# Optimization experiments

Hardware: AMD Instinct MI355X
Metric: run time of the kernel (lower is better)

## Reference

```python
import jax, jax.numpy as jnp
import numpy as np

SCALE = 0.1
TEMP = 1.0
LN_EPS = 1e-6
NORM_EPS = 1e-12  # torch F.normalize eps

def setup_inputs() -> dict:
    key = jax.random.key(0)
    k1, = jax.random.split(key, 1)
    x = jax.random.normal(k1, (8192, 512), dtype=jnp.float32)
    gamma = jnp.ones((512,), dtype=jnp.float32)
    beta = jnp.zeros((512,), dtype=jnp.float32)
    return {"x": x, "gamma": gamma, "beta": beta}

def reference(x, gamma, beta):
    # L2-normalize rows (torch F.normalize semantics: x / max(||x||, eps))
    norm = jnp.maximum(jnp.linalg.norm(x, axis=1, keepdims=True), NORM_EPS)
    xn = x / norm                                   # [N, d]
    sim = (xn @ xn.T) / TEMP                        # [N, N]
    # dual_norm: row softmax + column softmax
    sim = jax.nn.softmax(sim, axis=1) + jax.nn.softmax(sim, axis=0)
    x_neg = sim @ x                                 # [N, d]
    y = x - SCALE * x_neg
    # LayerNorm over last dim, eps=1e-6
    mean = jnp.mean(y, axis=-1, keepdims=True)
    var = jnp.mean(jnp.square(y - mean), axis=-1, keepdims=True)
    out = (y - mean) * jax.lax.rsqrt(var + LN_EPS) * gamma + beta
    return out
```

## Files before the change

kernel.cpp:

```cpp
#include <hip/hip_runtime.h>
#include <math.h>

#define NN 8192
#define DD 512

constexpr float SCALE_C = 0.1f;
constexpr float LN_EPS_C = 1e-6f;
constexpr float NORM_EPS_C = 1e-12f;
constexpr float CBIG = 32768.0f;
constexpr float INV_CBIG = 1.0f / 32768.0f;

typedef __attribute__((ext_vector_type(8))) short bf16x8;
typedef __attribute__((ext_vector_type(4))) float f32x4;

#define MFMA16(a, b, c) __builtin_amdgcn_mfma_f32_16x16x32_bf16((a), (b), (c), 0, 0, 0)
#define MFMA8(a, b, c)                                                        \
  __builtin_amdgcn_mfma_f32_16x16x32_fp8_fp8((long)(a), (long)(b), (c), 0, 0, 0)

#define GLL16(g, l)                                                        \
  __builtin_amdgcn_global_load_lds(                                        \
      (const __attribute__((address_space(1))) unsigned int*)(g),          \
      (__attribute__((address_space(3))) unsigned int*)(l), 16, 0, 0)

#define WAITV4() asm volatile("s_waitcnt vmcnt(4)" ::: "memory")
#define WAITV0() asm volatile("s_waitcnt vmcnt(0)" ::: "memory")
#define WAITLGKM0() asm volatile("s_waitcnt lgkmcnt(0)" ::: "memory")
#define FENCE() asm volatile("" ::: "memory")
#define BAR() __builtin_amdgcn_s_barrier()

__device__ inline unsigned short f2bf(float f) {
  unsigned int u = __builtin_bit_cast(unsigned int, f);
  unsigned int r = (u + 0x7FFFu + ((u >> 16) & 1u)) >> 16;
  return (unsigned short)r;
}

__device__ inline unsigned int f2fp8n(float f) {
  unsigned int a = __builtin_bit_cast(unsigned int, f);
  unsigned int r = a + 0x7FFFFu + ((a >> 20) & 1u);
  return (r >> 20) - 960u;
}

__device__ inline unsigned int f2fp8(float f) {
  unsigned int u = __builtin_bit_cast(unsigned int, f);
  unsigned int s = (u >> 24) & 0x80u;
  unsigned int a = u & 0x7fffffffu;
  if (a >= 0x3C800000u) {
    unsigned int r = a + 0x7FFFFu + ((a >> 20) & 1u);
    return s | ((r >> 20) - 960u);
  }
  float af = __builtin_bit_cast(float, a);
  return s | (unsigned int)(int)rintf(af * 512.0f);
}

__device__ inline float fp82f(unsigned int b) {
  return __builtin_bit_cast(float, (b + 960u) << 20);
}

__global__ __launch_bounds__(128) void k_prep(const float* __restrict__ x,
                                              unsigned short* __restrict__ xnb) {
  const int row = blockIdx.x;
  const int t = threadIdx.x;
  float4 v = ((const float4*)(x + (size_t)row * DD))[t];
  float ss = v.x * v.x + v.y * v.y + v.z * v.z + v.w * v.w;
#pragma unroll
  for (int off = 32; off; off >>= 1) ss += __shfl_down(ss, off);
  __shared__ float red[2];
  if ((t & 63) == 0) red[t >> 6] = ss;
  __syncthreads();
  float rn = 1.0f / fmaxf(sqrtf(red[0] + red[1]), NORM_EPS_C);
  ushort4 o;
  o.x = f2bf(v.x * rn);
  o.y = f2bf(v.y * rn);
  o.z = f2bf(v.z * rn);
  o.w = f2bf(v.w * rn);
  ((ushort4*)(xnb + (size_t)row * DD))[t] = o;
}

__global__ __launch_bounds__(256) void k_tr(const float* __restrict__ x,
                                            unsigned char* __restrict__ xT8) {
  __shared__ unsigned char T8[64][68];
  const int j0 = blockIdx.x * 64;
  const int d0 = blockIdx.y * 64;
  const int t = threadIdx.x;
#pragma unroll
  for (int q = 0; q < 4; ++q) {
    int f = t + q * 256;
    int r = f >> 4, c4 = f & 15;
    float4 v = *(const float4*)&x[(size_t)(j0 + r) * DD + d0 + c4 * 4];
    unsigned int w = f2fp8(v.x) | (f2fp8(v.y) << 8) | (f2fp8(v.z) << 16) |
                     (f2fp8(v.w) << 24);
    *(unsigned int*)&T8[r][c4 * 4] = w;
  }
  __syncthreads();
  {
    const int d = t >> 2, j16 = t & 3;
    unsigned int w[4];
#pragma unroll
    for (int p = 0; p < 4; ++p) {
      w[p] = (unsigned int)T8[j16 * 16 + p * 4 + 0][d] |
             ((unsigned int)T8[j16 * 16 + p * 4 + 1][d] << 8) |
             ((unsigned int)T8[j16 * 16 + p * 4 + 2][d] << 16) |
             ((unsigned int)T8[j16 * 16 + p * 4 + 3][d] << 24);
    }
    uint4 o = make_uint4(w[0], w[1], w[2], w[3]);
    *(uint4*)&xT8[(size_t)(d0 + d) * NN + j0 + j16 * 16] = o;
  }
}

__global__ __launch_bounds__(256, 4) void k_rowsumE(const unsigned short* __restrict__ xnb,
                                                    float* __restrict__ lpart,
                                                    unsigned char* __restrict__ E8) {
  __shared__ __align__(16) unsigned char POOL[36864];
  __shared__ float red[4][64];
  __shared__ float red2[4][64];

  int b = blockIdx.x, bi = 0;
  while (b >= 64 - bi) { b -= 64 - bi; ++bi; }
  const int bj = bi + b;
  const int i0 = bi * 128, j0 = bj * 128;
  const int diag = (bi == bj);

  const int t = threadIdx.x;
  const int w = t >> 6, l = t & 63;
  const int lr = l & 15, lg = l >> 4;
  const int wr = w >> 1, wc = w & 1;
  const int r0 = w * 16 + (l >> 2);
  const int clog = (l & 3) ^ ((r0 >> 1) & 3);
  const unsigned short* gA = xnb + (size_t)(i0 + r0) * DD + clog * 8;
  const unsigned short* gB = xnb + (size_t)(j0 + r0) * DD + clog * 8;

#define RS_STAGE(s, koff)                                                        \
  do {                                                                           \
    GLL16(gA + (koff), (unsigned short*)(POOL + (s) * 16384) + w * 512);         \
    GLL16(gA + (size_t)64 * DD + (koff),                                         \
          (unsigned short*)(POOL + (s) * 16384 + 4096) + w * 512);               \
    GLL16(gB + (koff), (unsigned short*)(POOL + (s) * 16384 + 8192) + w * 512);  \
    GLL16(gB + (size_t)64 * DD + (koff),                                         \
          (unsigned short*)(POOL + (s) * 16384 + 12288) + w * 512);              \
  } while (0)

  RS_STAGE(0, 0);
  RS_STAGE(1, 32);

  f32x4 acc[4][4] = {};
  for (int ks = 0; ks < 16; ++ks) {
    if (ks + 1 < 16) { WAITV4(); } else { WAITV0(); }
    BAR(); FENCE();
    const char* AS = (const char*)(POOL + (ks & 1) * 16384);
    const char* BS = AS + 8192;
    bf16x8 af[4], bv[4];
#pragma unroll
    for (int fm = 0; fm < 4; ++fm) {
      const int row = wr * 64 + fm * 16 + lr;
      af[fm] = *(const bf16x8*)(AS + row * 64 + ((lg ^ ((row >> 1) & 3)) << 4));
    }
#pragma unroll
    for (int fn = 0; fn < 4; ++fn) {
      const int row = wc * 64 + fn * 16 + lr;
      bv[fn] = *(const bf16x8*)(BS + row * 64 + ((lg ^ ((row >> 1) & 3)) << 4));
    }
    WAITLGKM0();
    BAR(); FENCE();
    if (ks + 2 < 16) RS_STAGE(ks & 1, (size_t)(ks + 2) * 32);
#pragma unroll
    for (int fm = 0; fm < 4; ++fm)
#pragma unroll
      for (int fn = 0; fn < 4; ++fn)
        acc[fm][fn] = MFMA16(af[fm], bv[fn], acc[fm][fn]);
  }

  unsigned int ebw[4][4];
  float rsum[4][4] = {};
  float csum[4] = {};
#pragma unroll
  for (int fm = 0; fm < 4; ++fm)
#pragma unroll
    for (int fn = 0; fn < 4; ++fn) {
      unsigned int pw = 0;
#pragma unroll
      for (int rr = 0; rr < 4; ++rr) {
        float e = __expf(acc[fm][fn][rr]);
        rsum[fm][rr] += e;
        csum[fn] += e;
        pw |= f2fp8n(e) << (8 * rr);
      }
      ebw[fm][fn] = pw;
    }

#pragma unroll
  for (int fm = 0; fm < 4; ++fm)
#pragma unroll
    for (int rr = 0; rr < 4; ++rr) {
      float s = rsum[fm][rr];
#pragma unroll
      for (int off = 1; off < 16; off <<= 1) s += __shfl_xor(s, off);
      if (lr == 0) red[w][fm * 16 + lg * 4 + rr] = s;
    }
  if (!diag) {
#pragma unroll
    for (int fn = 0; fn < 4; ++fn) {
      float cs = csum[fn];
      cs += __shfl_xor(cs, 16);
      cs += __shfl_xor(cs, 32);
      if (lg == 0) red2[w][fn * 16 + lr] = cs;
    }
  }

  unsigned char(*Et)[144] = (unsigned char(*)[144])POOL;
  unsigned char(*Et2)[144] = (unsigned char(*)[144])(POOL + 18432);
#pragma unroll
  for (int fm = 0; fm < 4; ++fm)
#pragma unroll
    for (int fn = 0; fn < 4; ++fn) {
#pragma unroll
      for (int rr = 0; rr < 4; ++rr)
        Et[wr * 64 + fm * 16 + lg * 4 + rr][wc * 64 + fn * 16 + lr] =
            (unsigned char)((ebw[fm][fn] >> (8 * rr)) & 0xffu);
      if (!diag)
        *(unsigned int*)&Et2[wc * 64 + fn * 16 + lr][wr * 64 + fm * 16 + lg * 4] =
            ebw[fm][fn];
    }
  __syncthreads();
  {
    unsigned char* dst = E8 + ((size_t)(bi * 64 + bj) << 14);
#pragma unroll
    for (int q = 0; q < 4; ++q) {
      const int f = t + q * 256;
      *(uint4*)(dst + f * 16) = *(const uint4*)&Et[f >> 3][(f & 7) * 16];
    }
    if (!diag) {
      unsigned char* dst2 = E8 + ((size_t)(bj * 64 + bi) << 14);
#pragma unroll
      for (int q = 0; q < 4; ++q) {
        const int f = t + q * 256;
        *(uint4*)(dst2 + f * 16) = *(const uint4*)&Et2[f >> 3][(f & 7) * 16];
      }
    }
  }
  if (t < 128) {
    const int wrx = t >> 6, idx = t & 63;
    lpart[(size_t)bj * NN + i0 + t] = red[2 * wrx][idx] + red[2 * wrx + 1][idx];
  } else if (!diag) {
    const int c = t - 128;
    const int wcx = c >> 6, idx = c & 63;
    lpart[(size_t)bi * NN + j0 + c] = red2[wcx][idx] + red2[2 + wcx][idx];
  }
}

__global__ __launch_bounds__(256) void k_recip(const float* __restrict__ lpart,
                                               float* __restrict__ rl) {
  const int i = blockIdx.x * 256 + threadIdx.x;
  float s = 0.f;
  for (int c = 0; c < 64; ++c) s += lpart[(size_t)c * NN + i];
  rl[i] = CBIG / s;
}

__global__ __launch_bounds__(256) void k_scale(unsigned char* __restrict__ P,
                                               const float* __restrict__ rl) {
  const long long total = (long long)NN * NN / 16;
  const long long stride = (long long)gridDim.x * 256;
  for (long long u = (long long)blockIdx.x * 256 + threadIdx.x; u < total; u += stride) {
    const long long byte = u * 16;
    const int tile = (int)(byte >> 14);
    const int within = (int)(byte & 16383);
    const int i = ((tile >> 6) << 7) + (within >> 7);
    const int j0 = ((tile & 63) << 7) + (within & 127);
    unsigned char* p = P + byte;
    uint4 v = *(const uint4*)p;
    const float rli = rl[i];
    float rlj[16];
#pragma unroll
    for (int q = 0; q < 4; ++q) {
      float4 r4 = *(const float4*)(rl + j0 + q * 4);
      rlj[q * 4 + 0] = r4.x; rlj[q * 4 + 1] = r4.y;
      rlj[q * 4 + 2] = r4.z; rlj[q * 4 + 3] = r4.w;
    }
    unsigned int wsrc[4] = {v.x, v.y, v.z, v.w};
    unsigned int wdst[4];
#pragma unroll
    for (int q = 0; q < 4; ++q) {
      unsigned int in = wsrc[q], out = 0;
#pragma unroll
      for (int k = 0; k < 4; ++k) {
        float e = fp82f((in >> (8 * k)) & 0xffu);
        out |= f2fp8n(e * (rli + rlj[q * 4 + k])) << (8 * k);
      }
      wdst[q] = out;
    }
    *(uint4*)p = make_uint4(wdst[0], wdst[1], wdst[2], wdst[3]);
  }
}

__global__ __launch_bounds__(256, 4) void k_pv3(const unsigned char* __restrict__ P8,
                                                const unsigned char* __restrict__ xT8,
                                                unsigned short* __restrict__ parts) {
  __shared__ __align__(16) unsigned char As[2][8192];
  __shared__ __align__(16) unsigned char Bs[2][8192];
  const int i0 = blockIdx.x * 128;
  const int n0 = blockIdx.y * 128;
  const int z = blockIdx.z;
  const int t = threadIdx.x;
  const int w = t >> 6, l = t & 63;
  const int lr = l & 15, lg = l >> 4;
  const int wr = w >> 1, wc = w & 1;
  const int r0 = w * 16 + (l >> 2);
  const int clog = (l & 3) ^ ((r0 >> 1) & 3);
  const unsigned char* Abase = P8 + ((size_t)((i0 >> 7) * 64 + z * 16) << 14) +
                               r0 * 128 + clog * 16;
  const unsigned char* gB = xT8 + (size_t)(n0 + r0) * NN + z * 2048 + clog * 16;

#define PV_STAGE(s, koff)                                                      \
  do {                                                                         \
    const unsigned char* a_ = Abase + (((koff) >> 7) << 14) + ((koff) & 127);  \
    GLL16(a_, &As[s][w * 1024]);                                               \
    GLL16(a_ + 8192, &As[s][4096 + w * 1024]);                                 \
    GLL16(gB + (koff), &Bs[s][w * 1024]);                                      \
    GLL16(gB + (size_t)64 * NN + (koff), &Bs[s][4096 + w * 1024]);             \
  } while (0)

  PV_STAGE(0, 0);
  PV_STAGE(1, 64);

  f32x4 acc[4][4] = {};
  for (int ks = 0; ks < 32; ++ks) {
    if (ks + 1 < 32) { WAITV4(); } else { WAITV0(); }
    BAR(); FENCE();
    const char* AS = (const char*)&As[ks & 1][0];
    const char* BS = (const char*)&Bs[ks & 1][0];
    unsigned long long af[4][2], bv[4][2];
#pragma unroll
    for (int fm = 0; fm < 4; ++fm) {
      const int row = wr * 64 + fm * 16 + lr;
      const int swz = (row >> 1) & 3;
#pragma unroll
      for (int kk = 0; kk < 2; ++kk) {
        int off = row * 64 + (((kk * 2 + (lg >> 1)) ^ swz) << 4) + ((lg & 1) << 3);
        af[fm][kk] = *(const unsigned long long*)(AS + off);
      }
    }
#pragma unroll
    for (int fn = 0; fn < 4; ++fn) {
      const int row = wc * 64 + fn * 16 + lr;
      const int swz = (row >> 1) & 3;
#pragma unroll
      for (int kk = 0; kk < 2; ++kk) {
        int off = row * 64 + (((kk * 2 + (lg >> 1)) ^ swz) << 4) + ((lg & 1) << 3);
        bv[fn][kk] = *(const unsigned long long*)(BS + off);
      }
    }
    WAITLGKM0();
    BAR(); FENCE();
    if (ks + 2 < 32) PV_STAGE(ks & 1, (ks + 2) * 64);
#pragma unroll
    for (int kk = 0; kk < 2; ++kk)
#pragma unroll
      for (int fm = 0; fm < 4; ++fm)
#pragma unroll
        for (int fn = 0; fn < 4; ++fn)
          acc[fm][fn] = MFMA8(af[fm][kk], bv[fn][kk], acc[fm][fn]);
  }
  unsigned short* dst = parts + (size_t)z * NN * DD;
#pragma unroll
  for (int fm = 0; fm < 4; ++fm)
#pragma unroll
    for (int fn = 0; fn < 4; ++fn)
#pragma unroll
      for (int rr = 0; rr < 4; ++rr)
        dst[(size_t)(i0 + wr * 64 + fm * 16 + lg * 4 + rr) * DD + n0 + wc * 64 +
            fn * 16 + lr] = f2bf(acc[fm][fn][rr] * INV_CBIG);
}

__global__ __launch_bounds__(128) void k_ln(const float* __restrict__ x,
                                            float* __restrict__ out,
                                            const unsigned short* __restrict__ parts,
                                            const float* __restrict__ gamma,
                                            const float* __restrict__ beta) {
  const int row = blockIdx.x;
  const int t = threadIdx.x;
  float4 p = make_float4(0.f, 0.f, 0.f, 0.f);
#pragma unroll
  for (int s = 0; s < 4; ++s) {
    ushort4 q = ((const ushort4*)(parts + (size_t)s * NN * DD + (size_t)row * DD))[t];
    p.x += __builtin_bit_cast(float, (unsigned int)q.x << 16);
    p.y += __builtin_bit_cast(float, (unsigned int)q.y << 16);
    p.z += __builtin_bit_cast(float, (unsigned int)q.z << 16);
    p.w += __builtin_bit_cast(float, (unsigned int)q.w << 16);
  }
  float4 xv = ((const float4*)(x + (size_t)row * DD))[t];
  float4 y;
  y.x = xv.x - SCALE_C * p.x;
  y.y = xv.y - SCALE_C * p.y;
  y.z = xv.z - SCALE_C * p.z;
  y.w = xv.w - SCALE_C * p.w;
  float sum = y.x + y.y + y.z + y.w;
#pragma unroll
  for (int off = 32; off; off >>= 1) sum += __shfl_down(sum, off);
  __shared__ float ra[2], rb[2];
  if ((t & 63) == 0) ra[t >> 6] = sum;
  __syncthreads();
  float mean = (ra[0] + ra[1]) * (1.0f / DD);
  float d0 = y.x - mean, d1 = y.y - mean, d2 = y.z - mean, d3 = y.w - mean;
  float vs = d0 * d0 + d1 * d1 + d2 * d2 + d3 * d3;
#pragma unroll
  for (int off = 32; off; off >>= 1) vs += __shfl_down(vs, off);
  if ((t & 63) == 0) rb[t >> 6] = vs;
  __syncthreads();
  float rstd = rsqrtf((rb[0] + rb[1]) * (1.0f / DD) + LN_EPS_C);
  float4 g4 = ((const float4*)gamma)[t];
  float4 b4 = ((const float4*)beta)[t];
  float4 o;
  o.x = d0 * rstd * g4.x + b4.x;
  o.y = d1 * rstd * g4.y + b4.y;
  o.z = d2 * rstd * g4.z + b4.z;
  o.w = d3 * rstd * g4.w + b4.w;
  ((float4*)(out + (size_t)row * DD))[t] = o;
}

extern "C" void kernel_launch(void* const* d_in, const int* in_sizes, int n_in,
                              void* d_out, int out_size, void* d_ws, size_t ws_size,
                              hipStream_t stream) {
  const float* x = (const float*)d_in[0];
  const float* gamma = (const float*)d_in[1];
  const float* beta = (const float*)d_in[2];
  float* out = (float*)d_out;

  unsigned short* xnb = (unsigned short*)d_ws;
  unsigned char* xT8 = (unsigned char*)(xnb + (size_t)NN * DD);
  float* lpart = (float*)(xT8 + (size_t)NN * DD);
  float* rl = lpart + (size_t)64 * NN;
  unsigned short* parts = (unsigned short*)(rl + NN);
  unsigned char* E8 = (unsigned char*)(parts + (size_t)4 * NN * DD);

  k_prep<<<NN, 128, 0, stream>>>(x, xnb);
  k_tr<<<dim3(NN / 64, DD / 64), 256, 0, stream>>>(x, xT8);
  k_rowsumE<<<2080, 256, 0, stream>>>(xnb, lpart, E8);
  k_recip<<<NN / 256, 256, 0, stream>>>(lpart, rl);
  k_scale<<<4096, 256, 0, stream>>>(E8, rl);
  k_pv3<<<dim3(64, 4, 4), 256, 0, stream>>>(E8, xT8, parts);
  k_ln<<<NN, 128, 0, stream>>>(x, out, parts, gamma, beta);
}
```

Baseline: 162.8 us.

## Triple-buffer LDS pipeline with one barrier per step, MFMA priority, block swizzle

```diff
diff --git a/kernel.cpp b/kernel.cpp
--- a/kernel.cpp
+++ b/kernel.cpp
@@ -24,7 +24,6 @@
 
 #define WAITV4() asm volatile("s_waitcnt vmcnt(4)" ::: "memory")
 #define WAITV0() asm volatile("s_waitcnt vmcnt(0)" ::: "memory")
-#define WAITLGKM0() asm volatile("s_waitcnt lgkmcnt(0)" ::: "memory")
 #define FENCE() asm volatile("" ::: "memory")
 #define BAR() __builtin_amdgcn_s_barrier()
 
@@ -107,14 +106,15 @@
   }
 }
 
-__global__ __launch_bounds__(256, 4) void k_rowsumE(const unsigned short* __restrict__ xnb,
+__global__ __launch_bounds__(256, 3) void k_rowsumE(const unsigned short* __restrict__ xnb,
                                                     float* __restrict__ lpart,
                                                     unsigned char* __restrict__ E8) {
-  __shared__ __align__(16) unsigned char POOL[36864];
+  __shared__ __align__(16) unsigned char POOL[49152];
   __shared__ float red[4][64];
   __shared__ float red2[4][64];
 
-  int b = blockIdx.x, bi = 0;
+  int b = (blockIdx.x & 7) * 260 + (blockIdx.x >> 3);
+  int bi = 0;
   while (b >= 64 - bi) { b -= 64 - bi; ++bi; }
   const int bj = bi + b;
   const int i0 = bi * 128, j0 = bj * 128;
@@ -144,9 +144,11 @@
 
   f32x4 acc[4][4] = {};
   for (int ks = 0; ks < 16; ++ks) {
-    if (ks + 1 < 16) { WAITV4(); } else { WAITV0(); }
+    WAITV4();
     BAR(); FENCE();
-    const char* AS = (const char*)(POOL + (ks & 1) * 16384);
+    const int kn = (ks + 2 < 16) ? ks + 2 : 15;
+    RS_STAGE((ks + 2) % 3, (size_t)kn * 32);
+    const char* AS = (const char*)(POOL + (ks % 3) * 16384);
     const char* BS = AS + 8192;
     bf16x8 af[4], bv[4];
 #pragma unroll
@@ -159,15 +161,15 @@
       const int row = wc * 64 + fn * 16 + lr;
       bv[fn] = *(const bf16x8*)(BS + row * 64 + ((lg ^ ((row >> 1) & 3)) << 4));
     }
-    WAITLGKM0();
-    BAR(); FENCE();
-    if (ks + 2 < 16) RS_STAGE(ks & 1, (size_t)(ks + 2) * 32);
+    __builtin_amdgcn_s_setprio(1);
 #pragma unroll
     for (int fm = 0; fm < 4; ++fm)
 #pragma unroll
       for (int fn = 0; fn < 4; ++fn)
         acc[fm][fn] = MFMA16(af[fm], bv[fn], acc[fm][fn]);
-  }
+    __builtin_amdgcn_s_setprio(0);
+  }
+  BAR(); FENCE();
 
   unsigned int ebw[4][4];
   float rsum[4][4] = {};
@@ -291,11 +293,10 @@
   }
 }
 
-__global__ __launch_bounds__(256, 4) void k_pv3(const unsigned char* __restrict__ P8,
+__global__ __launch_bounds__(256, 3) void k_pv3(const unsigned char* __restrict__ P8,
                                                 const unsigned char* __restrict__ xT8,
                                                 unsigned short* __restrict__ parts) {
-  __shared__ __align__(16) unsigned char As[2][8192];
-  __shared__ __align__(16) unsigned char Bs[2][8192];
+  __shared__ __align__(16) unsigned char POOL[49152];
   const int i0 = blockIdx.x * 128;
   const int n0 = blockIdx.y * 128;
   const int z = blockIdx.z;
@@ -312,10 +313,11 @@
 #define PV_STAGE(s, koff)                                                      \
   do {                                                                         \
     const unsigned char* a_ = Abase + (((koff) >> 7) << 14) + ((koff) & 127);  \
-    GLL16(a_, &As[s][w * 1024]);                                               \
-    GLL16(a_ + 8192, &As[s][4096 + w * 1024]);                                 \
-    GLL16(gB + (koff), &Bs[s][w * 1024]);                                      \
-    GLL16(gB + (size_t)64 * NN + (koff), &Bs[s][4096 + w * 1024]);             \
+    unsigned char* ls_ = POOL + (s) * 16384;                                   \
+    GLL16(a_, ls_ + w * 1024);                                                 \
+    GLL16(a_ + 8192, ls_ + 4096 + w * 1024);                                   \
+    GLL16(gB + (koff), ls_ + 8192 + w * 1024);                                 \
+    GLL16(gB + (size_t)64 * NN + (koff), ls_ + 12288 + w * 1024);              \
   } while (0)
 
   PV_STAGE(0, 0);
@@ -323,10 +325,12 @@
 
   f32x4 acc[4][4] = {};
   for (int ks = 0; ks < 32; ++ks) {
-    if (ks + 1 < 32) { WAITV4(); } else { WAITV0(); }
+    WAITV4();
     BAR(); FENCE();
-    const char* AS = (const char*)&As[ks & 1][0];
-    const char* BS = (const char*)&Bs[ks & 1][0];
+    const int kn = (ks + 2 < 32) ? ks + 2 : 31;
+    PV_STAGE((ks + 2) % 3, kn * 64);
+    const char* AS = (const char*)(POOL + (ks % 3) * 16384);
+    const char* BS = AS + 8192;
     unsigned long long af[4][2], bv[4][2];
 #pragma unroll
     for (int fm = 0; fm < 4; ++fm) {
@@ -348,9 +352,7 @@
         bv[fn][kk] = *(const unsigned long long*)(BS + off);
       }
     }
-    WAITLGKM0();
-    BAR(); FENCE();
-    if (ks + 2 < 32) PV_STAGE(ks & 1, (ks + 2) * 64);
+    __builtin_amdgcn_s_setprio(1);
 #pragma unroll
     for (int kk = 0; kk < 2; ++kk)
 #pragma unroll
@@ -358,6 +360,7 @@
 #pragma unroll
         for (int fn = 0; fn < 4; ++fn)
           acc[fm][fn] = MFMA8(af[fm][kk], bv[fn][kk], acc[fm][fn]);
+    __builtin_amdgcn_s_setprio(0);
   }
   unsigned short* dst = parts + (size_t)z * NN * DD;
 #pragma unroll
```

After: 172.0 us. 5.6% more time.

## Write only upper-triangle exp tiles and mirror transposes during scaling pass

Applied to the files above, without the earlier changes.

```diff
diff --git a/kernel.cpp b/kernel.cpp
--- a/kernel.cpp
+++ b/kernel.cpp
@@ -110,7 +110,7 @@
 __global__ __launch_bounds__(256, 4) void k_rowsumE(const unsigned short* __restrict__ xnb,
                                                     float* __restrict__ lpart,
                                                     unsigned char* __restrict__ E8) {
-  __shared__ __align__(16) unsigned char POOL[36864];
+  __shared__ __align__(16) unsigned char POOL[32768];
   __shared__ float red[4][64];
   __shared__ float red2[4][64];
 
@@ -207,7 +207,6 @@
   }
 
   unsigned char(*Et)[144] = (unsigned char(*)[144])POOL;
-  unsigned char(*Et2)[144] = (unsigned char(*)[144])(POOL + 18432);
 #pragma unroll
   for (int fm = 0; fm < 4; ++fm)
 #pragma unroll
@@ -216,9 +215,6 @@
       for (int rr = 0; rr < 4; ++rr)
         Et[wr * 64 + fm * 16 + lg * 4 + rr][wc * 64 + fn * 16 + lr] =
             (unsigned char)((ebw[fm][fn] >> (8 * rr)) & 0xffu);
-      if (!diag)
-        *(unsigned int*)&Et2[wc * 64 + fn * 16 + lr][wr * 64 + fm * 16 + lg * 4] =
-            ebw[fm][fn];
     }
   __syncthreads();
   {
@@ -227,14 +223,6 @@
     for (int q = 0; q < 4; ++q) {
       const int f = t + q * 256;
       *(uint4*)(dst + f * 16) = *(const uint4*)&Et[f >> 3][(f & 7) * 16];
-    }
-    if (!diag) {
-      unsigned char* dst2 = E8 + ((size_t)(bj * 64 + bi) << 14);
-#pragma unroll
-      for (int q = 0; q < 4; ++q) {
-        const int f = t + q * 256;
-        *(uint4*)(dst2 + f * 16) = *(const uint4*)&Et2[f >> 3][(f & 7) * 16];
-      }
     }
   }
   if (t < 128) {
@@ -255,39 +243,73 @@
   rl[i] = CBIG / s;
 }
 
-__global__ __launch_bounds__(256) void k_scale(unsigned char* __restrict__ P,
-                                               const float* __restrict__ rl) {
-  const long long total = (long long)NN * NN / 16;
-  const long long stride = (long long)gridDim.x * 256;
-  for (long long u = (long long)blockIdx.x * 256 + threadIdx.x; u < total; u += stride) {
-    const long long byte = u * 16;
-    const int tile = (int)(byte >> 14);
-    const int within = (int)(byte & 16383);
-    const int i = ((tile >> 6) << 7) + (within >> 7);
-    const int j0 = ((tile & 63) << 7) + (within & 127);
-    unsigned char* p = P + byte;
-    uint4 v = *(const uint4*)p;
-    const float rli = rl[i];
+__global__ __launch_bounds__(256) void k_scale2(unsigned char* __restrict__ P,
+                                                const float* __restrict__ rl) {
+  __shared__ unsigned int T32[128][35];
+  int b = blockIdx.x, ti = 0;
+  while (b >= 64 - ti) { b -= 64 - ti; ++ti; }
+  const int tj = ti + b;
+  const int i0 = ti * 128, j0 = tj * 128;
+  const int t = threadIdx.x;
+  unsigned char* tileC = P + ((size_t)(ti * 64 + tj) << 14);
+
+#pragma unroll
+  for (int q = 0; q < 4; ++q) {
+    const int f = t + q * 256;
+    const int r = f >> 3;
+    const int c0 = (f & 7) * 16;
+    uint4 v = *(const uint4*)(tileC + f * 16);
+    const float rli = rl[i0 + r];
     float rlj[16];
 #pragma unroll
-    for (int q = 0; q < 4; ++q) {
-      float4 r4 = *(const float4*)(rl + j0 + q * 4);
-      rlj[q * 4 + 0] = r4.x; rlj[q * 4 + 1] = r4.y;
-      rlj[q * 4 + 2] = r4.z; rlj[q * 4 + 3] = r4.w;
+    for (int p = 0; p < 4; ++p) {
+      float4 r4 = *(const float4*)(rl + j0 + c0 + p * 4);
+      rlj[p * 4 + 0] = r4.x; rlj[p * 4 + 1] = r4.y;
+      rlj[p * 4 + 2] = r4.z; rlj[p * 4 + 3] = r4.w;
     }
     unsigned int wsrc[4] = {v.x, v.y, v.z, v.w};
     unsigned int wdst[4];
 #pragma unroll
-    for (int q = 0; q < 4; ++q) {
-      unsigned int in = wsrc[q], out = 0;
+    for (int p = 0; p < 4; ++p) {
+      unsigned int in = wsrc[p], out = 0;
 #pragma unroll
       for (int k = 0; k < 4; ++k) {
         float e = fp82f((in >> (8 * k)) & 0xffu);
-        out |= f2fp8n(e * (rli + rlj[q * 4 + k])) << (8 * k);
+        out |= f2fp8n(e * (rli + rlj[p * 4 + k])) << (8 * k);
       }
-      wdst[q] = out;
-    }
-    *(uint4*)p = make_uint4(wdst[0], wdst[1], wdst[2], wdst[3]);
+      wdst[p] = out;
+      T32[r][(c0 >> 2) + p] = out;
+    }
+    *(uint4*)(tileC + f * 16) = make_uint4(wdst[0], wdst[1], wdst[2], wdst[3]);
+  }
+  if (ti == tj) return;
+  __syncthreads();
+
+  unsigned char* tileT = P + ((size_t)(tj * 64 + ti) << 14);
+  {
+    const int rg = t >> 3;
+    const int cc = t & 7;
+    const int c2 = cc * 16;
+    unsigned int o[4][4];
+#pragma unroll
+    for (int k4 = 0; k4 < 4; ++k4) {
+      unsigned int a0 = T32[c2 + k4 * 4 + 0][rg];
+      unsigned int a1 = T32[c2 + k4 * 4 + 1][rg];
+      unsigned int a2 = T32[c2 + k4 * 4 + 2][rg];
+      unsigned int a3 = T32[c2 + k4 * 4 + 3][rg];
+      unsigned int b0 = (a0 & 0x00FF00FFu) | ((a1 << 8) & 0xFF00FF00u);
+      unsigned int b1 = ((a0 >> 8) & 0x00FF00FFu) | (a1 & 0xFF00FF00u);
+      unsigned int b2 = (a2 & 0x00FF00FFu) | ((a3 << 8) & 0xFF00FF00u);
+      unsigned int b3 = ((a2 >> 8) & 0x00FF00FFu) | (a3 & 0xFF00FF00u);
+      o[0][k4] = (b0 & 0x0000FFFFu) | (b2 << 16);
+      o[1][k4] = (b1 & 0x0000FFFFu) | (b3 << 16);
+      o[2][k4] = (b0 >> 16) | (b2 & 0xFFFF0000u);
+      o[3][k4] = (b1 >> 16) | (b3 & 0xFFFF0000u);
+    }
+#pragma unroll
+    for (int i = 0; i < 4; ++i)
+      *(uint4*)(tileT + (size_t)(rg * 4 + i) * 128 + c2) =
+          make_uint4(o[i][0], o[i][1], o[i][2], o[i][3]);
   }
 }
 
@@ -435,7 +457,7 @@
   k_tr<<<dim3(NN / 64, DD / 64), 256, 0, stream>>>(x, xT8);
   k_rowsumE<<<2080, 256, 0, stream>>>(xnb, lpart, E8);
   k_recip<<<NN / 256, 256, 0, stream>>>(lpart, rl);
-  k_scale<<<4096, 256, 0, stream>>>(E8, rl);
+  k_scale2<<<2080, 256, 0, stream>>>(E8, rl);
   k_pv3<<<dim3(64, 4, 4), 256, 0, stream>>>(E8, xT8, parts);
   k_ln<<<NN, 128, 0, stream>>>(x, out, parts, gamma, beta);
 }
```

Result: faster. 153.8 us (-5.5%).
